# Kernel tuning notes

Measured on AMD Instinct MI355X. Metric: run time of the kernel, lower is better.

## Reference

```python
import jax, jax.numpy as jnp
import numpy as np

B = 131072      # number of graphs
P = 22          # num_players (pad/truncate target)
F = 14          # num_features
N = B * P       # total nodes
H1, H2 = 256, 128


def setup_inputs() -> dict:
    key = jax.random.key(0)
    ks = jax.random.split(key, 8)
    x = jax.random.normal(ks[0], (N, F), dtype=jnp.float32)
    batch = jnp.sort(jax.random.randint(ks[1], (N,), 0, B, dtype=jnp.int32))
    s1 = 1.0 / np.sqrt(P * F)
    s2 = 1.0 / np.sqrt(H1)
    s3 = 1.0 / np.sqrt(H2)
    W1 = jax.random.uniform(ks[2], (H1, P * F), jnp.float32, -s1, s1)
    b1 = jax.random.uniform(ks[3], (H1,), jnp.float32, -s1, s1)
    W2 = jax.random.uniform(ks[4], (H2, H1), jnp.float32, -s2, s2)
    b2 = jax.random.uniform(ks[5], (H2,), jnp.float32, -s2, s2)
    W3 = jax.random.uniform(ks[6], (P, H2), jnp.float32, -s3, s3)
    b3 = jax.random.uniform(ks[7], (P,), jnp.float32, -s3, s3)
    return {"x": x, "batch": batch, "W1": W1, "b1": b1, "W2": W2, "b2": b2, "W3": W3, "b3": b3}


def _flatten_batch(x, batch):
    # Vectorized equivalent of the per-graph mask/slice/pad loop.
    counts = jax.ops.segment_sum(jnp.ones((N,), jnp.int32), batch, num_segments=B)
    starts = jnp.concatenate([jnp.zeros((1,), jnp.int32), jnp.cumsum(counts)[:-1].astype(jnp.int32)])
    pos = jnp.arange(N, dtype=jnp.int32) - starts[batch]  # position within own graph
    # nodes beyond the first P per graph are truncated -> route to dump slot P
    slot = jnp.where(pos < P, pos, P)
    buf = jnp.zeros((B, P + 1, F), dtype=x.dtype)          # zero padding for short graphs
    buf = buf.at[batch, slot].set(x)
    return buf[:, :P, :].reshape(B, P * F)


def reference(x, batch, W1, b1, W2, b2, W3, b3):
    flat = _flatten_batch(x, batch)                        # [B, 308]
    h1 = jax.nn.relu(flat @ W1.T + b1)                     # dropout is eval-mode identity
    h2 = jax.nn.relu(h1 @ W2.T + b2)
    logits = h2 @ W3.T + b3                                # [B, 22]
    return logits
```

## Files before the change

### kernel.cpp

```cpp
#include <hip/hip_runtime.h>
#include <hip/hip_fp16.h>

typedef __attribute__((ext_vector_type(8))) _Float16 half8;
typedef __attribute__((ext_vector_type(4))) float f32x4;

namespace {
constexpr int B_G = 131072;
constexpr int P   = 22;
constexpr int F   = 14;
constexpr int NF  = 308;
constexpr long long N_NODES = (long long)B_G * P;

constexpr int G    = 64;
constexpr int NBLK = B_G / G;

constexpr int KS1 = 10;
constexpr int KS2 = 8;
constexpr int KS3 = 4;
constexpr int JT1 = 16;
constexpr int JT2 = 8;
constexpr int JT3 = 2;

constexpr int W1F = 0;
constexpr int W2F = W1F + KS1 * JT1 * 1024;
constexpr int W3F = W2F + KS2 * JT2 * 1024;
constexpr int CVT_DWORDS = (KS1*JT1 + KS2*JT2 + KS3*JT3) * 256;
}

__device__ __forceinline__ unsigned short f2h(float v) {
    __half h = __float2half(v);
    return *reinterpret_cast<unsigned short*>(&h);
}

__global__ void convert_w_kernel(const float* __restrict__ W1,
                                 const float* __restrict__ W2,
                                 const float* __restrict__ W3,
                                 unsigned* __restrict__ ws)
{
    int p = blockIdx.x * 256 + threadIdx.x;
    if (p >= CVT_DWORDS) return;
    const int n1 = KS1 * JT1 * 256;
    const int n2 = KS2 * JT2 * 256;
    const float* W; int NK, NJ, stride, JT, oB, pl;
    if (p < n1)            { W = W1; NK = NF;  NJ = 256; stride = NF;  JT = JT1; oB = W1F/4; pl = p; }
    else if (p < n1 + n2)  { W = W2; NK = 256; NJ = 128; stride = 256; JT = JT2; oB = W2F/4; pl = p - n1; }
    else                   { W = W3; NK = 128; NJ = 22;  stride = 128; JT = JT3; oB = W3F/4; pl = p - n1 - n2; }

    const int e2   = pl & 3;
    const int lane = (pl >> 2) & 63;
    const int jt   = (pl >> 8) % JT;
    const int ks   = (pl >> 8) / JT;
    const int j    = jt * 16 + (lane & 15);
    const int kb   = ks * 32 + (lane >> 4) * 8 + e2 * 2;

    unsigned d = 0;
    #pragma unroll
    for (int q = 0; q < 2; ++q) {
        const int k = kb + q;
        const float v = (k < NK && j < NJ) ? W[j * stride + k] : 0.0f;
        d |= (unsigned)f2h(v) << (16 * q);
    }
    ws[oB + pl] = d;
}

#define MFMA16(A_, B_, C_) __builtin_amdgcn_mfma_f32_16x16x32_f16(A_, B_, C_, 0, 0, 0)

#define LOADB1(H_, KS_) { \
    _Pragma("unroll") for (int n = 0; n < 4; ++n) \
        H_[n] = *reinterpret_cast<const half8*>(&B1[((((KS_) * JT1) + (wv * 4 + n)) * 64 + lane) * 8]); }

#define COMP1(H_, KS_) { \
    half8 a_[4]; \
    _Pragma("unroll") for (int m = 0; m < 4; ++m) \
        a_[m] = *reinterpret_cast<const half8*>(&s_scr[(((KS_) * 4 + kq) * G + (m * 16 + r16)) * 8]); \
    _Pragma("unroll") for (int n = 0; n < 4; ++n) \
        _Pragma("unroll") for (int m = 0; m < 4; ++m) \
            acc[m][n] = MFMA16(a_[m], H_[n], acc[m][n]); }

#define LOADB2(H_, KS_) { \
    _Pragma("unroll") for (int n = 0; n < 2; ++n) \
        H_[n] = *reinterpret_cast<const half8*>(&B2[((((KS_) * JT2) + (wv * 2 + n)) * 64 + lane) * 8]); }

#define COMP2(H_, KS_) { \
    half8 a_[4]; \
    _Pragma("unroll") for (int m = 0; m < 4; ++m) \
        a_[m] = *reinterpret_cast<const half8*>(&s_scr[(((KS_) * 4 + kq) * G + (m * 16 + r16)) * 8]); \
    _Pragma("unroll") for (int n = 0; n < 2; ++n) \
        _Pragma("unroll") for (int m = 0; m < 4; ++m) \
            acc2[m][n] = MFMA16(a_[m], H_[n], acc2[m][n]); }

__global__ __launch_bounds__(256, 3)
void mlp_mfma_kernel(const float* __restrict__ x,
                     const int* __restrict__ batch,
                     const float* __restrict__ b1,
                     const float* __restrict__ b2,
                     const float* __restrict__ b3,
                     const unsigned short* __restrict__ ws,
                     float* __restrict__ out)
{
    __shared__ __align__(16) unsigned short s_scr[24576];
    __shared__ float s_b1[256], s_b2[128], s_b3[32];
    __shared__ int s_start[G + 1];

    const int t    = threadIdx.x;
    const int g0   = blockIdx.x * G;
    const int lane = t & 63;
    const int wv   = t >> 6;
    const int r16  = lane & 15;
    const int kq   = lane >> 4;

    if (t < 256) s_b1[t] = b1[t];
    if (t < 128) s_b2[t] = b2[t];
    if (t < 32)  s_b3[t] = (t < 22) ? b3[t] : 0.0f;

    if (t <= G) {
        const int target = g0 + t;
        long long wl = (long long)target * P - 5001; if (wl < 0) wl = 0;
        long long wh = (long long)target * P + 5001; if (wh > N_NODES) wh = N_NODES;
        int lo = (int)wl, hi = (int)wh;
        while (lo < hi) { int mid = (lo + hi) >> 1; if (batch[mid] < target) lo = mid + 1; else hi = mid; }
        const bool ok = (lo == 0 || batch[lo - 1] < target) &&
                        (lo == (int)N_NODES || batch[lo] >= target);
        if (!ok) {
            lo = 0; hi = (int)N_NODES;
            while (lo < hi) { int mid = (lo + hi) >> 1; if (batch[mid] < target) lo = mid + 1; else hi = mid; }
        }
        s_start[t] = lo;
    }

    for (int i = t; i < 2560; i += 256)
        reinterpret_cast<uint4*>(s_scr)[i] = make_uint4(0u, 0u, 0u, 0u);
    __syncthreads();

    const int s0 = s_start[0], s1 = s_start[G];
    for (int i = s0 + t; i < s1; i += 256) {
        const int gl = batch[i] - g0;
        const int pp = i - s_start[gl];
        if (pp < P) {
            const float2* xr = reinterpret_cast<const float2*>(x + (size_t)i * F);
            #pragma unroll
            for (int q = 0; q < 7; ++q) {
                const float2 v = xr[q];
                const int k = pp * F + q * 2;
                const unsigned d = (unsigned)f2h(v.x) | ((unsigned)f2h(v.y) << 16);
                const int off = (((k >> 5) * 4 + ((k >> 3) & 3)) * G + gl) * 8 + (k & 7);
                *reinterpret_cast<unsigned*>(&s_scr[off]) = d;
            }
        }
    }

    const unsigned short* B1 = ws + W1F / 2;
    const unsigned short* B2 = ws + W2F / 2;
    const unsigned short* B3 = ws + W3F / 2;

    half8 Ba[4], Bb[4], Bc[4];
    LOADB1(Ba, 0)
    LOADB1(Bb, 1)
    __syncthreads();

    f32x4 acc[4][4];
    #pragma unroll
    for (int m = 0; m < 4; ++m)
        #pragma unroll
        for (int n = 0; n < 4; ++n) acc[m][n] = (f32x4){0.f, 0.f, 0.f, 0.f};

    LOADB1(Bc, 2)  COMP1(Ba, 0)
    LOADB1(Ba, 3)  COMP1(Bb, 1)
    LOADB1(Bb, 4)  COMP1(Bc, 2)
    LOADB1(Bc, 5)  COMP1(Ba, 3)
    LOADB1(Ba, 6)  COMP1(Bb, 4)
    LOADB1(Bb, 7)  COMP1(Bc, 5)
    LOADB1(Bc, 8)  COMP1(Ba, 6)
    LOADB1(Ba, 9)  COMP1(Bb, 7)
    COMP1(Bc, 8)

    half8 Ca[2], Cb[2], Cc[2];
    LOADB2(Ca, 0)
    LOADB2(Cb, 1)
    COMP1(Ba, 9)
    __syncthreads();

    #pragma unroll
    for (int n = 0; n < 4; ++n) {
        const int j = (wv * 4 + n) * 16 + r16;
        const float bb = s_b1[j];
        const int base = (((j >> 5) * 4 + ((j >> 3) & 3)) * G) * 8 + (j & 7);
        #pragma unroll
        for (int m = 0; m < 4; ++m)
            #pragma unroll
            for (int r = 0; r < 4; ++r) {
                const int g = m * 16 + kq * 4 + r;
                s_scr[base + g * 8] = f2h(fmaxf(acc[m][n][r] + bb, 0.0f));
            }
    }
    __syncthreads();

    f32x4 acc2[4][2];
    #pragma unroll
    for (int m = 0; m < 4; ++m)
        #pragma unroll
        for (int n = 0; n < 2; ++n) acc2[m][n] = (f32x4){0.f, 0.f, 0.f, 0.f};

    LOADB2(Cc, 2)  COMP2(Ca, 0)
    LOADB2(Ca, 3)  COMP2(Cb, 1)
    LOADB2(Cb, 4)  COMP2(Cc, 2)
    LOADB2(Cc, 5)  COMP2(Ca, 3)
    LOADB2(Ca, 6)  COMP2(Cb, 4)
    LOADB2(Cb, 7)  COMP2(Cc, 5)
    COMP2(Ca, 6)

    half8 D3[8];
    #pragma unroll
    for (int ks = 0; ks < KS3; ++ks)
        #pragma unroll
        for (int n = 0; n < 2; ++n)
            D3[ks * 2 + n] = *reinterpret_cast<const half8*>(&B3[((ks * JT3 + n) * 64 + lane) * 8]);
    COMP2(Cb, 7)

    #pragma unroll
    for (int n = 0; n < 2; ++n) {
        const int j = (wv * 2 + n) * 16 + r16;
        const float bb = s_b2[j];
        const int base = 16384 + (((j >> 5) * 4 + ((j >> 3) & 3)) * G) * 8 + (j & 7);
        #pragma unroll
        for (int m = 0; m < 4; ++m)
            #pragma unroll
            for (int r = 0; r < 4; ++r) {
                const int g = m * 16 + kq * 4 + r;
                s_scr[base + g * 8] = f2h(fmaxf(acc2[m][n][r] + bb, 0.0f));
            }
    }
    __syncthreads();

    {
        f32x4 acc3[2];
        acc3[0] = (f32x4){0.f, 0.f, 0.f, 0.f};
        acc3[1] = (f32x4){0.f, 0.f, 0.f, 0.f};
        #pragma unroll
        for (int ks = 0; ks < KS3; ++ks) {
            const half8 a = *reinterpret_cast<const half8*>(
                &s_scr[16384 + ((ks * 4 + kq) * G + (wv * 16 + r16)) * 8]);
            #pragma unroll
            for (int n = 0; n < 2; ++n)
                acc3[n] = MFMA16(a, D3[ks * 2 + n], acc3[n]);
        }
        #pragma unroll
        for (int n = 0; n < 2; ++n) {
            const int j = n * 16 + r16;
            if (j < P) {
                const float bb = s_b3[j];
                #pragma unroll
                for (int r = 0; r < 4; ++r) {
                    const int g = wv * 16 + kq * 4 + r;
                    out[(size_t)(g0 + g) * P + j] = acc3[n][r] + bb;
                }
            }
        }
    }
}

extern "C" void kernel_launch(void* const* d_in, const int* in_sizes, int n_in,
                              void* d_out, int out_size, void* d_ws, size_t ws_size,
                              hipStream_t stream) {
    const float* x     = (const float*)d_in[0];
    const int*   batch = (const int*)  d_in[1];
    const float* W1    = (const float*)d_in[2];
    const float* b1    = (const float*)d_in[3];
    const float* W2    = (const float*)d_in[4];
    const float* b2    = (const float*)d_in[5];
    const float* W3    = (const float*)d_in[6];
    const float* b3    = (const float*)d_in[7];
    float* out = (float*)d_out;

    convert_w_kernel<<<dim3((CVT_DWORDS + 255) / 256), dim3(256), 0, stream>>>(
        W1, W2, W3, (unsigned*)d_ws);
    mlp_mfma_kernel<<<dim3(NBLK), dim3(256), 0, stream>>>(
        x, batch, b1, b2, b3, (const unsigned short*)d_ws, out);
}
```

Before: 69.37 us.

## Use 512-thread blocks with 8 waves splitting MLP output columns

Doubles the threads per block from 256 to 512, so each of the 8 waves owns half as many output column tiles in every layer. Per-wave accumulators and weight fragments shrink, and launch bounds rise to 6 blocks per CU. The aim is more waves in flight to hide memory latency and lower register pressure. In exchange, each A fragment loaded from LDS feeds fewer MFMAs, so LDS traffic per MFMA doubles. LDS usage per block (about 49KB) may also cap how many blocks actually co-reside.

After: 80.88 us. +16.6%, slower.

```diff
diff --git a/kernel.cpp b/kernel.cpp
--- a/kernel.cpp
+++ b/kernel.cpp
@@ -13,6 +13,7 @@
 
 constexpr int G    = 64;
 constexpr int NBLK = B_G / G;
+constexpr int NT   = 512;
 
 constexpr int KS1 = 10;
 constexpr int KS2 = 8;
@@ -66,30 +67,28 @@
 #define MFMA16(A_, B_, C_) __builtin_amdgcn_mfma_f32_16x16x32_f16(A_, B_, C_, 0, 0, 0)
 
 #define LOADB1(H_, KS_) { \
-    _Pragma("unroll") for (int n = 0; n < 4; ++n) \
-        H_[n] = *reinterpret_cast<const half8*>(&B1[((((KS_) * JT1) + (wv * 4 + n)) * 64 + lane) * 8]); }
+    _Pragma("unroll") for (int n = 0; n < 2; ++n) \
+        H_[n] = *reinterpret_cast<const half8*>(&B1[((((KS_) * JT1) + (wv * 2 + n)) * 64 + lane) * 8]); }
 
 #define COMP1(H_, KS_) { \
-    half8 a_[4]; \
-    _Pragma("unroll") for (int m = 0; m < 4; ++m) \
-        a_[m] = *reinterpret_cast<const half8*>(&s_scr[(((KS_) * 4 + kq) * G + (m * 16 + r16)) * 8]); \
-    _Pragma("unroll") for (int n = 0; n < 4; ++n) \
-        _Pragma("unroll") for (int m = 0; m < 4; ++m) \
-            acc[m][n] = MFMA16(a_[m], H_[n], acc[m][n]); }
-
-#define LOADB2(H_, KS_) { \
-    _Pragma("unroll") for (int n = 0; n < 2; ++n) \
-        H_[n] = *reinterpret_cast<const half8*>(&B2[((((KS_) * JT2) + (wv * 2 + n)) * 64 + lane) * 8]); }
-
-#define COMP2(H_, KS_) { \
     half8 a_[4]; \
     _Pragma("unroll") for (int m = 0; m < 4; ++m) \
         a_[m] = *reinterpret_cast<const half8*>(&s_scr[(((KS_) * 4 + kq) * G + (m * 16 + r16)) * 8]); \
     _Pragma("unroll") for (int n = 0; n < 2; ++n) \
         _Pragma("unroll") for (int m = 0; m < 4; ++m) \
-            acc2[m][n] = MFMA16(a_[m], H_[n], acc2[m][n]); }
-
-__global__ __launch_bounds__(256, 3)
+            acc[m][n] = MFMA16(a_[m], H_[n], acc[m][n]); }
+
+#define LOADB2(H_, KS_) { \
+    H_ = *reinterpret_cast<const half8*>(&B2[((((KS_) * JT2) + wv) * 64 + lane) * 8]); }
+
+#define COMP2(H_, KS_) { \
+    half8 a_[4]; \
+    _Pragma("unroll") for (int m = 0; m < 4; ++m) \
+        a_[m] = *reinterpret_cast<const half8*>(&s_scr[(((KS_) * 4 + kq) * G + (m * 16 + r16)) * 8]); \
+    _Pragma("unroll") for (int m = 0; m < 4; ++m) \
+        acc2[m] = MFMA16(a_[m], H_, acc2[m]); }
+
+__global__ __launch_bounds__(NT, 6)
 void mlp_mfma_kernel(const float* __restrict__ x,
                      const int* __restrict__ batch,
                      const float* __restrict__ b1,
@@ -128,12 +127,12 @@
         s_start[t] = lo;
     }
 
-    for (int i = t; i < 2560; i += 256)
+    for (int i = t; i < 2560; i += NT)
         reinterpret_cast<uint4*>(s_scr)[i] = make_uint4(0u, 0u, 0u, 0u);
     __syncthreads();
 
     const int s0 = s_start[0], s1 = s_start[G];
-    for (int i = s0 + t; i < s1; i += 256) {
+    for (int i = s0 + t; i < s1; i += NT) {
         const int gl = batch[i] - g0;
         const int pp = i - s_start[gl];
         if (pp < P) {
@@ -153,16 +152,16 @@
     const unsigned short* B2 = ws + W2F / 2;
     const unsigned short* B3 = ws + W3F / 2;
 
-    half8 Ba[4], Bb[4], Bc[4];
+    half8 Ba[2], Bb[2], Bc[2];
     LOADB1(Ba, 0)
     LOADB1(Bb, 1)
     __syncthreads();
 
-    f32x4 acc[4][4];
+    f32x4 acc[4][2];
     #pragma unroll
     for (int m = 0; m < 4; ++m)
         #pragma unroll
-        for (int n = 0; n < 4; ++n) acc[m][n] = (f32x4){0.f, 0.f, 0.f, 0.f};
+        for (int n = 0; n < 2; ++n) acc[m][n] = (f32x4){0.f, 0.f, 0.f, 0.f};
 
     LOADB1(Bc, 2)  COMP1(Ba, 0)
     LOADB1(Ba, 3)  COMP1(Bb, 1)
@@ -174,15 +173,15 @@
     LOADB1(Ba, 9)  COMP1(Bb, 7)
     COMP1(Bc, 8)
 
-    half8 Ca[2], Cb[2], Cc[2];
+    half8 Ca, Cb, Cc;
     LOADB2(Ca, 0)
     LOADB2(Cb, 1)
     COMP1(Ba, 9)
     __syncthreads();
 
     #pragma unroll
-    for (int n = 0; n < 4; ++n) {
-        const int j = (wv * 4 + n) * 16 + r16;
+    for (int n = 0; n < 2; ++n) {
+        const int j = (wv * 2 + n) * 16 + r16;
         const float bb = s_b1[j];
         const int base = (((j >> 5) * 4 + ((j >> 3) & 3)) * G) * 8 + (j & 7);
         #pragma unroll
@@ -195,11 +194,9 @@
     }
     __syncthreads();
 
-    f32x4 acc2[4][2];
-    #pragma unroll
-    for (int m = 0; m < 4; ++m)
-        #pragma unroll
-        for (int n = 0; n < 2; ++n) acc2[m][n] = (f32x4){0.f, 0.f, 0.f, 0.f};
+    f32x4 acc2[4];
+    #pragma unroll
+    for (int m = 0; m < 4; ++m) acc2[m] = (f32x4){0.f, 0.f, 0.f, 0.f};
 
     LOADB2(Cc, 2)  COMP2(Ca, 0)
     LOADB2(Ca, 3)  COMP2(Cb, 1)
@@ -209,17 +206,14 @@
     LOADB2(Cb, 7)  COMP2(Cc, 5)
     COMP2(Ca, 6)
 
-    half8 D3[8];
+    half8 D3[4];
     #pragma unroll
     for (int ks = 0; ks < KS3; ++ks)
-        #pragma unroll
-        for (int n = 0; n < 2; ++n)
-            D3[ks * 2 + n] = *reinterpret_cast<const half8*>(&B3[((ks * JT3 + n) * 64 + lane) * 8]);
+        D3[ks] = *reinterpret_cast<const half8*>(&B3[((ks * JT3 + (wv & 1)) * 64 + lane) * 8]);
     COMP2(Cb, 7)
 
-    #pragma unroll
-    for (int n = 0; n < 2; ++n) {
-        const int j = (wv * 2 + n) * 16 + r16;
+    {
+        const int j = wv * 16 + r16;
         const float bb = s_b2[j];
         const int base = 16384 + (((j >> 5) * 4 + ((j >> 3) & 3)) * G) * 8 + (j & 7);
         #pragma unroll
@@ -227,33 +221,27 @@
             #pragma unroll
             for (int r = 0; r < 4; ++r) {
                 const int g = m * 16 + kq * 4 + r;
-                s_scr[base + g * 8] = f2h(fmaxf(acc2[m][n][r] + bb, 0.0f));
+                s_scr[base + g * 8] = f2h(fmaxf(acc2[m][r] + bb, 0.0f));
             }
     }
     __syncthreads();
 
     {
-        f32x4 acc3[2];
-        acc3[0] = (f32x4){0.f, 0.f, 0.f, 0.f};
-        acc3[1] = (f32x4){0.f, 0.f, 0.f, 0.f};
+        f32x4 acc3 = (f32x4){0.f, 0.f, 0.f, 0.f};
+        const int mg = (wv >> 1) * 16;
         #pragma unroll
         for (int ks = 0; ks < KS3; ++ks) {
             const half8 a = *reinterpret_cast<const half8*>(
-                &s_scr[16384 + ((ks * 4 + kq) * G + (wv * 16 + r16)) * 8]);
-            #pragma unroll
-            for (int n = 0; n < 2; ++n)
-                acc3[n] = MFMA16(a, D3[ks * 2 + n], acc3[n]);
-        }
-        #pragma unroll
-        for (int n = 0; n < 2; ++n) {
-            const int j = n * 16 + r16;
-            if (j < P) {
-                const float bb = s_b3[j];
-                #pragma unroll
-                for (int r = 0; r < 4; ++r) {
-                    const int g = wv * 16 + kq * 4 + r;
-                    out[(size_t)(g0 + g) * P + j] = acc3[n][r] + bb;
-                }
+                &s_scr[16384 + ((ks * 4 + kq) * G + (mg + r16)) * 8]);
+            acc3 = MFMA16(a, D3[ks], acc3);
+        }
+        const int j = (wv & 1) * 16 + r16;
+        if (j < P) {
+            const float bb = s_b3[j];
+            #pragma unroll
+            for (int r = 0; r < 4; ++r) {
+                const int g = mg + kq * 4 + r;
+                out[(size_t)(g0 + g) * P + j] = acc3[r] + bb;
             }
         }
     }
@@ -274,6 +262,6 @@
 
     convert_w_kernel<<<dim3((CVT_DWORDS + 255) / 256), dim3(256), 0, stream>>>(
         W1, W2, W3, (unsigned*)d_ws);
-    mlp_mfma_kernel<<<dim3(NBLK), dim3(256), 0, stream>>>(
+    mlp_mfma_kernel<<<dim3(NBLK), dim3(NT), 0, stream>>>(
         x, batch, b1, b2, b3, (const unsigned short*)d_ws, out);
 }
```

## Prefetch weight fragments before gather, unroll gather loop, reorder MFMA/load pipeline

Applied to the files above, without the earlier changes.

Issues the first three W1 fragment loads before the node gather and merges the zero-fill and gather barriers, so global weight loads overlap with the scatter of x into shared memory. The gather loop is unrolled seven times to expose more independent loads, and empty asm statements pin the prefetched registers. The steady-state schedule now issues each compute before the next load, and the first layer-2 fragments are prefetched earlier. This raises register pressure under the 3-blocks-per-CU launch bound and could cause spills or lower occupancy.

Measured after the change: 68.43 us. Within noise of the previous version (-1.4%).

```diff
diff --git a/kernel.cpp b/kernel.cpp
--- a/kernel.cpp
+++ b/kernel.cpp
@@ -89,6 +89,22 @@
         _Pragma("unroll") for (int m = 0; m < 4; ++m) \
             acc2[m][n] = MFMA16(a_[m], H_[n], acc2[m][n]); }
 
+#define GATHER_BODY(I_) { \
+    const int gl = batch[I_] - g0; \
+    const int pp = (I_) - s_start[gl]; \
+    if (pp < P) { \
+        const float2* xr = reinterpret_cast<const float2*>(x + (size_t)(I_) * F); \
+        _Pragma("unroll") for (int q = 0; q < 7; ++q) { \
+            const float2 v = xr[q]; \
+            const int k = pp * F + q * 2; \
+            const unsigned d = (unsigned)f2h(v.x) | ((unsigned)f2h(v.y) << 16); \
+            const int off = (((k >> 5) * 4 + ((k >> 3) & 3)) * G + gl) * 8 + (k & 7); \
+            *reinterpret_cast<unsigned*>(&s_scr[off]) = d; \
+        } \
+    } }
+
+#define PIN8(V_) asm volatile("" :: "v"(V_))
+
 __global__ __launch_bounds__(256, 3)
 void mlp_mfma_kernel(const float* __restrict__ x,
                      const int* __restrict__ batch,
@@ -109,7 +125,7 @@
     const int r16  = lane & 15;
     const int kq   = lane >> 4;
 
-    if (t < 256) s_b1[t] = b1[t];
+    s_b1[t] = b1[t];
     if (t < 128) s_b2[t] = b2[t];
     if (t < 32)  s_b3[t] = (t < 22) ? b3[t] : 0.0f;
 
@@ -130,24 +146,6 @@
 
     for (int i = t; i < 2560; i += 256)
         reinterpret_cast<uint4*>(s_scr)[i] = make_uint4(0u, 0u, 0u, 0u);
-    __syncthreads();
-
-    const int s0 = s_start[0], s1 = s_start[G];
-    for (int i = s0 + t; i < s1; i += 256) {
-        const int gl = batch[i] - g0;
-        const int pp = i - s_start[gl];
-        if (pp < P) {
-            const float2* xr = reinterpret_cast<const float2*>(x + (size_t)i * F);
-            #pragma unroll
-            for (int q = 0; q < 7; ++q) {
-                const float2 v = xr[q];
-                const int k = pp * F + q * 2;
-                const unsigned d = (unsigned)f2h(v.x) | ((unsigned)f2h(v.y) << 16);
-                const int off = (((k >> 5) * 4 + ((k >> 3) & 3)) * G + gl) * 8 + (k & 7);
-                *reinterpret_cast<unsigned*>(&s_scr[off]) = d;
-            }
-        }
-    }
 
     const unsigned short* B1 = ws + W1F / 2;
     const unsigned short* B2 = ws + W2F / 2;
@@ -156,6 +154,21 @@
     half8 Ba[4], Bb[4], Bc[4];
     LOADB1(Ba, 0)
     LOADB1(Bb, 1)
+    LOADB1(Bc, 2)
+    __syncthreads();
+
+    const int s0 = s_start[0], s1 = s_start[G];
+    #pragma unroll
+    for (int u = 0; u < 7; ++u) {
+        const int i = s0 + t + u * 256;
+        if (i < s1) GATHER_BODY(i)
+    }
+    for (int i = s0 + t + 7 * 256; i < s1; i += 256)
+        GATHER_BODY(i)
+
+    PIN8(Ba[0]); PIN8(Ba[1]); PIN8(Ba[2]); PIN8(Ba[3]);
+    PIN8(Bb[0]); PIN8(Bb[1]); PIN8(Bb[2]); PIN8(Bb[3]);
+    PIN8(Bc[0]); PIN8(Bc[1]); PIN8(Bc[2]); PIN8(Bc[3]);
     __syncthreads();
 
     f32x4 acc[4][4];
@@ -164,19 +177,20 @@
         #pragma unroll
         for (int n = 0; n < 4; ++n) acc[m][n] = (f32x4){0.f, 0.f, 0.f, 0.f};
 
-    LOADB1(Bc, 2)  COMP1(Ba, 0)
-    LOADB1(Ba, 3)  COMP1(Bb, 1)
-    LOADB1(Bb, 4)  COMP1(Bc, 2)
-    LOADB1(Bc, 5)  COMP1(Ba, 3)
-    LOADB1(Ba, 6)  COMP1(Bb, 4)
-    LOADB1(Bb, 7)  COMP1(Bc, 5)
-    LOADB1(Bc, 8)  COMP1(Ba, 6)
-    LOADB1(Ba, 9)  COMP1(Bb, 7)
-    COMP1(Bc, 8)
+    COMP1(Ba, 0)  LOADB1(Ba, 3)
+    COMP1(Bb, 1)  LOADB1(Bb, 4)
+    COMP1(Bc, 2)  LOADB1(Bc, 5)
+    COMP1(Ba, 3)  LOADB1(Ba, 6)
+    COMP1(Bb, 4)  LOADB1(Bb, 7)
+    COMP1(Bc, 5)  LOADB1(Bc, 8)
+    COMP1(Ba, 6)  LOADB1(Ba, 9)
+    COMP1(Bb, 7)
 
     half8 Ca[2], Cb[2], Cc[2];
     LOADB2(Ca, 0)
     LOADB2(Cb, 1)
+    LOADB2(Cc, 2)
+    COMP1(Bc, 8)
     COMP1(Ba, 9)
     __syncthreads();
 
@@ -201,12 +215,12 @@
         #pragma unroll
         for (int n = 0; n < 2; ++n) acc2[m][n] = (f32x4){0.f, 0.f, 0.f, 0.f};
 
-    LOADB2(Cc, 2)  COMP2(Ca, 0)
-    LOADB2(Ca, 3)  COMP2(Cb, 1)
-    LOADB2(Cb, 4)  COMP2(Cc, 2)
-    LOADB2(Cc, 5)  COMP2(Ca, 3)
-    LOADB2(Ca, 6)  COMP2(Cb, 4)
-    LOADB2(Cb, 7)  COMP2(Cc, 5)
+    COMP2(Ca, 0)  LOADB2(Ca, 3)
+    COMP2(Cb, 1)  LOADB2(Cb, 4)
+    COMP2(Cc, 2)  LOADB2(Cc, 5)
+    COMP2(Ca, 3)  LOADB2(Ca, 6)
+    COMP2(Cb, 4)  LOADB2(Cb, 7)
+    COMP2(Cc, 5)
     COMP2(Ca, 6)
 
     half8 D3[8];
```
